# Kernel tuning notes

Measured on AMD Instinct MI355X. Metric: run time of the kernel, lower is better.

Reference implementation:

```python
import jax, jax.numpy as jnp
import numpy as np

BETA = 0.25
EPS = 1e-12  # torch F.normalize eps


def _normalize(x):
    n = jnp.linalg.norm(x, axis=-1, keepdims=True)
    return x / jnp.maximum(n, EPS)


def setup_inputs() -> dict:
    key = jax.random.key(0)
    k1, k2 = jax.random.split(key)
    B, S, D, NE = 16, 2048, 512, 8192
    z = jax.random.normal(k1, (B, S, D), dtype=jnp.float32)
    emb = jax.random.normal(k2, (NE, D), dtype=jnp.float32)
    return {"z": z, "emb": emb}


def reference(z, emb):
    B, S, D = z.shape
    n_e = emb.shape[0]
    zf = z.reshape(-1, D)                      # [N, D]
    zn = _normalize(zf)
    embn = _normalize(emb)                     # [n_e, D]
    # squared euclidean distances: [N, n_e]
    d = (jnp.sum(zn * zn, axis=1, keepdims=True)
         + jnp.sum(embn * embn, axis=1)
         - 2.0 * jnp.matmul(zn, embn.T))
    idx = jnp.argmin(d, axis=1)                # [N]
    z_q = emb[idx].reshape(z.shape)            # raw codebook lookup (NOT normalized)
    # commitment / codebook loss on normalized vectors
    z_q_n = _normalize(z_q)
    z_n = _normalize(z)
    sg = jax.lax.stop_gradient
    loss = (jnp.mean((z_q_n - sg(z_n)) ** 2)
            + BETA * jnp.mean((sg(z_q_n) - z_n) ** 2))
    # straight-through estimator, then normalize
    z_q_st = z + sg(z_q - z)
    z_q_st = _normalize(z_q_st)
    # perplexity via usage counts (equivalent to mean of one-hots)
    N = zf.shape[0]
    counts = jnp.zeros((n_e,), dtype=z.dtype).at[idx].add(1.0)
    e_mean = counts / N
    perplexity = jnp.exp(-jnp.sum(e_mean * jnp.log(e_mean + 1e-10)))
    return loss, z_q_st, idx, perplexity
```

## Files before the change

### kernel.cpp

```cpp
#include <hip/hip_runtime.h>
#include <float.h>
#include <math.h>

#define DIM 512
#define EPSN 1e-12f

typedef _Float16 f16x8 __attribute__((ext_vector_type(8)));
typedef float f32x4 __attribute__((ext_vector_type(4)));

__device__ inline void gll16(const void* g, void* l) {
  __builtin_amdgcn_global_load_lds(
      (__attribute__((address_space(1))) void*)g,
      (__attribute__((address_space(3))) void*)l, 16, 0, 0);
}

__device__ inline float wave_sum(float v) {
#pragma unroll
  for (int o = 32; o > 0; o >>= 1) v += __shfl_xor(v, o, 64);
  return v;
}

__global__ __launch_bounds__(256) void emb_norm_kernel(
    const float* __restrict__ emb, float2* __restrict__ eepair) {
  int row = blockIdx.x * 4 + (threadIdx.x >> 6);
  int lane = threadIdx.x & 63;
  const float* p = emb + (size_t)row * DIM;
  float x[8];
  float ss = 0.f;
#pragma unroll
  for (int i = 0; i < 8; ++i) { x[i] = p[i * 64 + lane]; ss += x[i] * x[i]; }
  ss = wave_sum(ss);
  float d = fmaxf(sqrtf(ss), EPSN);
  float ee = 0.f;
#pragma unroll
  for (int i = 0; i < 8; ++i) { float y = x[i] / d; ee += y * y; }
  ee = wave_sum(ee);
  if (lane == 0) eepair[row] = make_float2(ee, 1.0f / d);
}

__global__ __launch_bounds__(256) void z_norm_kernel(
    const float* __restrict__ z, float* __restrict__ zinv) {
  int row = blockIdx.x * 4 + (threadIdx.x >> 6);
  int lane = threadIdx.x & 63;
  const float* p = z + (size_t)row * DIM;
  float ss = 0.f;
#pragma unroll
  for (int i = 0; i < 8; ++i) { float v = p[i * 64 + lane]; ss += v * v; }
  ss = wave_sum(ss);
  if (lane == 0) zinv[row] = 1.0f / fmaxf(sqrtf(ss), EPSN);
}

__global__ __launch_bounds__(256) void emb_split_kernel(
    const float* __restrict__ emb, _Float16* __restrict__ swz) {
  int g = blockIdx.x * 256 + threadIdx.x;
  int lane = g & 63;
  int kc = (g >> 6) & 15;
  int t = g >> 10;
  int code = t * 16 + (lane & 15);
  int k0 = kc * 32 + (lane >> 4) * 8;
  const float* src = emb + (size_t)code * DIM + k0;
  float4 a = *(const float4*)src;
  float4 b = *(const float4*)(src + 4);
  float v[8] = {a.x, a.y, a.z, a.w, b.x, b.y, b.z, b.w};
  f16x8 h, l;
#pragma unroll
  for (int k = 0; k < 8; ++k) {
    _Float16 hh = (_Float16)v[k];
    h[k] = hh;
    l[k] = (_Float16)(v[k] - (float)hh);
  }
  size_t cbase = ((size_t)(t * 16 + kc) * 2) * 512;
  *(f16x8*)&swz[cbase + lane * 8] = h;
  *(f16x8*)&swz[cbase + 512 + lane * 8] = l;
}

#define MFMA16(A, B, C) __builtin_amdgcn_mfma_f32_16x16x32_f16(A, B, C, 0, 0, 0)

__global__ __launch_bounds__(256, 1) void dist_argmin_kernel(
    const float* __restrict__ z, const _Float16* __restrict__ swz,
    const float2* __restrict__ eepair, const float* __restrict__ zinv,
    int ne, int* __restrict__ idxw, float* __restrict__ counts,
    float* __restrict__ out_idx) {
  __shared__ _Float16 B[2][32768];

  const int tid = threadIdx.x;
  const int wave = tid >> 6;
  const int lane = tid & 63;
  const int col = lane & 15;
  const int quad = lane >> 4;
  const int r0 = blockIdx.x * 128 + wave * 32;

  f16x8 Ah[2][16], Al[2][16];
#pragma unroll
  for (int rb = 0; rb < 2; ++rb) {
    const float* zp = z + (size_t)(r0 + rb * 16 + col) * DIM + quad * 8;
#pragma unroll
    for (int kc = 0; kc < 16; ++kc) {
      float4 a = *(const float4*)(zp + kc * 32);
      float4 b = *(const float4*)(zp + kc * 32 + 4);
      float v[8] = {a.x, a.y, a.z, a.w, b.x, b.y, b.z, b.w};
#pragma unroll
      for (int k = 0; k < 8; ++k) {
        _Float16 h = (_Float16)v[k];
        Ah[rb][kc][k] = h;
        Al[rb][kc][k] = (_Float16)(v[k] - (float)h);
      }
    }
  }

  float zr[2][4];
#pragma unroll
  for (int rb = 0; rb < 2; ++rb)
#pragma unroll
    for (int i = 0; i < 4; ++i)
      zr[rb][i] = zinv[r0 + rb * 16 + quad * 4 + i];

  float best[2][4] = {{FLT_MAX, FLT_MAX, FLT_MAX, FLT_MAX},
                      {FLT_MAX, FLT_MAX, FLT_MAX, FLT_MAX}};
  int bidx[2][4] = {{0, 0, 0, 0}, {0, 0, 0, 0}};

  const int ntiles = ne / 32;

  {
    const _Float16* g0 = swz + (size_t)(wave * 16) * 512 + lane * 8;
    _Float16* l0 = &B[0][(wave * 16) * 512 + lane * 8];
#pragma unroll
    for (int i = 0; i < 16; ++i)
      gll16(g0 + i * 512, l0 + i * 512);
  }
  __syncthreads();

  for (int t = 0; t < ntiles; ++t) {
    const int buf = t & 1;

    if (t + 1 < ntiles) {
      const _Float16* g0 =
          swz + ((size_t)(t + 1) * 64 + wave * 16) * 512 + lane * 8;
      _Float16* l0 = &B[buf ^ 1][(wave * 16) * 512 + lane * 8];
#pragma unroll
      for (int i = 0; i < 16; ++i)
        gll16(g0 + i * 512, l0 + i * 512);
    }

#pragma unroll
    for (int s = 0; s < 2; ++s) {
      const int n0 = (t * 2 + s) * 16;
      float2 ep = eepair[n0 + col];

      f32x4 acc[2][3];
#pragma unroll
      for (int rb = 0; rb < 2; ++rb)
#pragma unroll
        for (int a = 0; a < 3; ++a) acc[rb][a] = (f32x4){0.f, 0.f, 0.f, 0.f};

      const _Float16* bp = &B[buf][(s * 32) * 512 + lane * 8];
#pragma unroll
      for (int kc = 0; kc < 16; ++kc) {
        f16x8 bh = *(const f16x8*)(bp + (kc * 2) * 512);
        f16x8 bl = *(const f16x8*)(bp + (kc * 2 + 1) * 512);
        acc[0][0] = MFMA16(Ah[0][kc], bh, acc[0][0]);
        acc[1][0] = MFMA16(Ah[1][kc], bh, acc[1][0]);
        acc[0][1] = MFMA16(Al[0][kc], bh, acc[0][1]);
        acc[1][1] = MFMA16(Al[1][kc], bh, acc[1][1]);
        acc[0][2] = MFMA16(Ah[0][kc], bl, acc[0][2]);
        acc[1][2] = MFMA16(Ah[1][kc], bl, acc[1][2]);
      }

      float w2 = 2.0f * ep.y;
      int j = n0 + col;
#pragma unroll
      for (int rb = 0; rb < 2; ++rb)
#pragma unroll
        for (int i = 0; i < 4; ++i) {
          float d = acc[rb][0][i] + acc[rb][1][i] + acc[rb][2][i];
          float sc = ep.x - w2 * zr[rb][i] * d;
          if (sc < best[rb][i]) { best[rb][i] = sc; bidx[rb][i] = j; }
        }
    }
    __syncthreads();
  }

#pragma unroll
  for (int rb = 0; rb < 2; ++rb)
#pragma unroll
    for (int i = 0; i < 4; ++i) {
      float bs = best[rb][i];
      int bj = bidx[rb][i];
#pragma unroll
      for (int off = 1; off < 16; off <<= 1) {
        float os = __shfl_xor(bs, off, 64);
        int oi = __shfl_xor(bj, off, 64);
        if (os < bs || (os == bs && oi < bj)) { bs = os; bj = oi; }
      }
      if (col == 0) {
        int row = r0 + rb * 16 + quad * 4 + i;
        idxw[row] = bj;
        out_idx[row] = (float)bj;
        atomicAdd(&counts[bj], 1.0f);
      }
    }
}

__global__ __launch_bounds__(256) void finalize_rows_kernel(
    const float* __restrict__ z, const float* __restrict__ emb,
    const int* __restrict__ idxw, const float* __restrict__ zinv,
    float* __restrict__ out_zq, float* __restrict__ lpart) {
  __shared__ float red[4];
  int row = blockIdx.x * 4 + (threadIdx.x >> 6);
  int lane = threadIdx.x & 63;
  int j = idxw[row];
  const float* zp = z + (size_t)row * DIM;
  const float* qp = emb + (size_t)j * DIM;
  float zl[8], ql[8], tl[8];
  float st = 0.f, sq = 0.f;
#pragma unroll
  for (int i = 0; i < 8; ++i) {
    int k = i * 64 + lane;
    float zv = zp[k], qv = qp[k];
    float t = zv + (qv - zv);
    zl[i] = zv; ql[i] = qv; tl[i] = t;
    st += t * t;
    sq += qv * qv;
  }
  st = wave_sum(st);
  sq = wave_sum(sq);
  float dt = fmaxf(sqrtf(st), EPSN);
  float dq = fmaxf(sqrtf(sq), EPSN);
  float zi = zinv[row];
  float lp = 0.f;
#pragma unroll
  for (int i = 0; i < 8; ++i) {
    int k = i * 64 + lane;
    out_zq[(size_t)row * DIM + k] = tl[i] / dt;
    float e = ql[i] / dq - zl[i] * zi;
    lp += e * e;
  }
  lp = wave_sum(lp);
  if (lane == 0) red[threadIdx.x >> 6] = lp;
  __syncthreads();
  if (threadIdx.x == 0) lpart[blockIdx.x] = red[0] + red[1] + red[2] + red[3];
}

__global__ __launch_bounds__(256) void scalars_kernel(
    const float* __restrict__ counts, const float* __restrict__ lpart,
    int ne, int nblk, float inv_n, float inv_total,
    float* __restrict__ out_loss, float* __restrict__ out_perp) {
  __shared__ float red[8];
  int tid = threadIdx.x;
  float s = 0.f;
  for (int jj = tid; jj < ne; jj += 256) {
    float p = counts[jj] * inv_n;
    s += p * logf(p + 1e-10f);
  }
  float l = 0.f;
  for (int jj = tid; jj < nblk; jj += 256) l += lpart[jj];
  s = wave_sum(s);
  l = wave_sum(l);
  if ((tid & 63) == 0) { red[tid >> 6] = s; red[4 + (tid >> 6)] = l; }
  __syncthreads();
  if (tid == 0) {
    float t = red[0] + red[1] + red[2] + red[3];
    float lt = red[4] + red[5] + red[6] + red[7];
    *out_perp = expf(-t);
    *out_loss = 1.25f * lt * inv_total;
  }
}

extern "C" void kernel_launch(void* const* d_in, const int* in_sizes, int n_in,
                              void* d_out, int out_size, void* d_ws, size_t ws_size,
                              hipStream_t stream) {
  const float* z = (const float*)d_in[0];
  const float* emb = (const float*)d_in[1];
  float* out = (float*)d_out;
  float* ws = (float*)d_ws;

  const int nrows = in_sizes[0] / DIM;
  const int ne = in_sizes[1] / DIM;
  const int nfin = nrows / 4;

  float2* eepair = (float2*)ws;
  float* zinv = ws + 2 * ne;
  int* idxw = (int*)(ws + 2 * ne + nrows);
  float* counts = ws + 2 * ne + 2 * nrows;
  float* lpart = counts + ne;
  _Float16* swz = (_Float16*)(lpart + nfin);

  float* out_zq = out + 1;
  float* out_idx = out + 1 + (size_t)nrows * DIM;
  float* out_perp = out + (size_t)out_size - 1;

  hipMemsetAsync(counts, 0, ne * sizeof(float), stream);
  emb_norm_kernel<<<ne / 4, 256, 0, stream>>>(emb, eepair);
  z_norm_kernel<<<nrows / 4, 256, 0, stream>>>(z, zinv);
  emb_split_kernel<<<ne * 64 / 256, 256, 0, stream>>>(emb, swz);
  dist_argmin_kernel<<<nrows / 128, 256, 0, stream>>>(z, swz, eepair, zinv, ne,
                                                      idxw, counts, out_idx);
  finalize_rows_kernel<<<nfin, 256, 0, stream>>>(z, emb, idxw, zinv,
                                                 out_zq, lpart);
  scalars_kernel<<<1, 256, 0, stream>>>(counts, lpart, ne, nfin,
                                        1.0f / (float)nrows,
                                        1.0f / (float)((size_t)nrows * DIM),
                                        out, out_perp);
}
```

Measured before the change: 1.120 ms.

## Load codebook fragments directly from global memory instead of LDS double buffering

Removes the shared-memory double-buffered staging of the swizzled fp16 codebook (global_load_lds plus block barriers) and has each wave read its B fragments straight from global/L2 into registers, one 16-column subtile at a time. This drops the per-tile __syncthreads and the LDS traffic, so waves run independently. In exchange, all four waves in a block and every block re-read the same codebook from cache. The next subtile's loads are no longer prefetched, so latency hiding depends on the compiler and on occupancy, and register pressure rises with 32 f16x8 B fragments per iteration.

```diff
diff --git a/kernel.cpp b/kernel.cpp
--- a/kernel.cpp
+++ b/kernel.cpp
@@ -7,12 +7,6 @@
 
 typedef _Float16 f16x8 __attribute__((ext_vector_type(8)));
 typedef float f32x4 __attribute__((ext_vector_type(4)));
-
-__device__ inline void gll16(const void* g, void* l) {
-  __builtin_amdgcn_global_load_lds(
-      (__attribute__((address_space(1))) void*)g,
-      (__attribute__((address_space(3))) void*)l, 16, 0, 0);
-}
 
 __device__ inline float wave_sum(float v) {
 #pragma unroll
@@ -81,8 +75,6 @@
     const float2* __restrict__ eepair, const float* __restrict__ zinv,
     int ne, int* __restrict__ idxw, float* __restrict__ counts,
     float* __restrict__ out_idx) {
-  __shared__ _Float16 B[2][32768];
-
   const int tid = threadIdx.x;
   const int wave = tid >> 6;
   const int lane = tid & 63;
@@ -119,65 +111,45 @@
                       {FLT_MAX, FLT_MAX, FLT_MAX, FLT_MAX}};
   int bidx[2][4] = {{0, 0, 0, 0}, {0, 0, 0, 0}};
 
-  const int ntiles = ne / 32;
-
-  {
-    const _Float16* g0 = swz + (size_t)(wave * 16) * 512 + lane * 8;
-    _Float16* l0 = &B[0][(wave * 16) * 512 + lane * 8];
-#pragma unroll
-    for (int i = 0; i < 16; ++i)
-      gll16(g0 + i * 512, l0 + i * 512);
-  }
-  __syncthreads();
-
-  for (int t = 0; t < ntiles; ++t) {
-    const int buf = t & 1;
-
-    if (t + 1 < ntiles) {
-      const _Float16* g0 =
-          swz + ((size_t)(t + 1) * 64 + wave * 16) * 512 + lane * 8;
-      _Float16* l0 = &B[buf ^ 1][(wave * 16) * 512 + lane * 8];
-#pragma unroll
-      for (int i = 0; i < 16; ++i)
-        gll16(g0 + i * 512, l0 + i * 512);
-    }
-
-#pragma unroll
-    for (int s = 0; s < 2; ++s) {
-      const int n0 = (t * 2 + s) * 16;
-      float2 ep = eepair[n0 + col];
-
-      f32x4 acc[2][3];
-#pragma unroll
-      for (int rb = 0; rb < 2; ++rb)
-#pragma unroll
-        for (int a = 0; a < 3; ++a) acc[rb][a] = (f32x4){0.f, 0.f, 0.f, 0.f};
-
-      const _Float16* bp = &B[buf][(s * 32) * 512 + lane * 8];
-#pragma unroll
-      for (int kc = 0; kc < 16; ++kc) {
-        f16x8 bh = *(const f16x8*)(bp + (kc * 2) * 512);
-        f16x8 bl = *(const f16x8*)(bp + (kc * 2 + 1) * 512);
-        acc[0][0] = MFMA16(Ah[0][kc], bh, acc[0][0]);
-        acc[1][0] = MFMA16(Ah[1][kc], bh, acc[1][0]);
-        acc[0][1] = MFMA16(Al[0][kc], bh, acc[0][1]);
-        acc[1][1] = MFMA16(Al[1][kc], bh, acc[1][1]);
-        acc[0][2] = MFMA16(Ah[0][kc], bl, acc[0][2]);
-        acc[1][2] = MFMA16(Ah[1][kc], bl, acc[1][2]);
-      }
-
-      float w2 = 2.0f * ep.y;
-      int j = n0 + col;
-#pragma unroll
-      for (int rb = 0; rb < 2; ++rb)
-#pragma unroll
-        for (int i = 0; i < 4; ++i) {
-          float d = acc[rb][0][i] + acc[rb][1][i] + acc[rb][2][i];
-          float sc = ep.x - w2 * zr[rb][i] * d;
-          if (sc < best[rb][i]) { best[rb][i] = sc; bidx[rb][i] = j; }
-        }
-    }
-    __syncthreads();
+  const _Float16* bp = swz + lane * 8;
+  const int nsub = ne / 16;
+
+  for (int s = 0; s < nsub; ++s) {
+    f16x8 bh[16], bl[16];
+#pragma unroll
+    for (int kc = 0; kc < 16; ++kc) {
+      const _Float16* c0 = bp + ((size_t)(s * 16 + kc) * 2) * 512;
+      bh[kc] = *(const f16x8*)c0;
+      bl[kc] = *(const f16x8*)(c0 + 512);
+    }
+
+    f32x4 acc[2][3];
+#pragma unroll
+    for (int rb = 0; rb < 2; ++rb)
+#pragma unroll
+      for (int a = 0; a < 3; ++a) acc[rb][a] = (f32x4){0.f, 0.f, 0.f, 0.f};
+
+#pragma unroll
+    for (int kc = 0; kc < 16; ++kc) {
+      acc[0][0] = MFMA16(Ah[0][kc], bh[kc], acc[0][0]);
+      acc[1][0] = MFMA16(Ah[1][kc], bh[kc], acc[1][0]);
+      acc[0][1] = MFMA16(Al[0][kc], bh[kc], acc[0][1]);
+      acc[1][1] = MFMA16(Al[1][kc], bh[kc], acc[1][1]);
+      acc[0][2] = MFMA16(Ah[0][kc], bl[kc], acc[0][2]);
+      acc[1][2] = MFMA16(Ah[1][kc], bl[kc], acc[1][2]);
+    }
+
+    float2 ep = eepair[s * 16 + col];
+    float w2 = 2.0f * ep.y;
+    int j = s * 16 + col;
+#pragma unroll
+    for (int rb = 0; rb < 2; ++rb)
+#pragma unroll
+      for (int i = 0; i < 4; ++i) {
+        float d = acc[rb][0][i] + acc[rb][1][i] + acc[rb][2][i];
+        float sc = ep.x - w2 * zr[rb][i] * d;
+        if (sc < best[rb][i]) { best[rb][i] = sc; bidx[rb][i] = j; }
+      }
   }
 
 #pragma unroll
```

Measured after the change: 2.760 ms. 2.46x slower.
